# Kernel optimization log

Measured on AMD Instinct MI355X. Metric: run time of the kernel, lower is better.

The kernel has to match this reference:

```python
import jax, jax.numpy as jnp
import numpy as np

N = 100000   # nodes
E = 1600000  # edges
F = 128      # num_features
H = 128      # embedding_size
C = 10       # num_classes
G = 64       # graphs in batch


def setup_inputs() -> dict:
    key = jax.random.key(0)
    ks = jax.random.split(key, 10)
    x = jax.random.normal(ks[0], (N, F), jnp.float32)
    edge_index = jax.random.randint(ks[1], (2, E), 0, N)
    batch_index = jnp.sort(jax.random.randint(ks[2], (N,), 0, G))
    glorot = lambda k, shape: jax.random.normal(k, shape, jnp.float32) / np.float32(np.sqrt(shape[0]))
    return {
        "x": x, "edge_index": edge_index, "batch_index": batch_index,
        "W0": glorot(ks[3], (F, H)), "b0": jnp.zeros((H,), jnp.float32),
        "W1": glorot(ks[4], (H, H)), "b1": jnp.zeros((H,), jnp.float32),
        "W2": glorot(ks[5], (H, H)), "b2": jnp.zeros((H,), jnp.float32),
        "W3": glorot(ks[6], (H, H)), "b3": jnp.zeros((H,), jnp.float32),
        "Wout": glorot(ks[7], (2 * H, C)), "bout": jnp.zeros((C,), jnp.float32),
    }


def gcn_conv(x, W, b, src, dst):
    """PyG GCNConv: self-loops + symmetric D^-1/2 (A+I) D^-1/2 normalization."""
    n = x.shape[0]
    # degree with self-loop: deg[i] = 1 + in-degree(i)
    deg = 1.0 + jax.ops.segment_sum(jnp.ones(dst.shape[0], x.dtype), dst, num_segments=n)
    dinv = jax.lax.rsqrt(deg)
    h = x @ W  # [N, H]
    norm = (dinv[src] * dinv[dst])[:, None]  # [E, 1]
    agg = jax.ops.segment_sum(h[src] * norm, dst, num_segments=n)  # scatter-add over edges
    agg = agg + h * (1.0 / deg)[:, None]  # self-loop contribution dinv[i]^2 * h[i]
    return agg + b


def reference(x, edge_index, batch_index, W0, b0, W1, b1, W2, b2, W3, b3, Wout, bout):
    src, dst = edge_index[0], edge_index[1]
    h = jnp.tanh(gcn_conv(x, W0, b0, src, dst))
    h = jnp.tanh(gcn_conv(h, W1, b1, src, dst))
    h = jnp.tanh(gcn_conv(h, W2, b2, src, dst))
    h = jnp.tanh(gcn_conv(h, W3, b3, src, dst))
    # global max pool + global mean pool over batch_index
    gmax = jax.ops.segment_max(h, batch_index, num_segments=G)
    cnt = jax.ops.segment_sum(jnp.ones((h.shape[0],), h.dtype), batch_index, num_segments=G)
    gmean = jax.ops.segment_sum(h, batch_index, num_segments=G) / jnp.maximum(cnt, 1.0)[:, None]
    pooled = jnp.concatenate([gmax, gmean], axis=1)  # [G, 2H]
    out = pooled @ Wout + bout  # [G, C]
    return out, pooled
```

## Files before the change

kernel.cpp:

```cpp
#include <hip/hip_runtime.h>
#include <hip/hip_fp16.h>
#include <cmath>

typedef __attribute__((ext_vector_type(8))) short short8;
typedef __attribute__((ext_vector_type(8))) unsigned short ushort8;
typedef __attribute__((ext_vector_type(8))) _Float16 f16x8;
typedef __attribute__((ext_vector_type(4))) float f32x4;

#define MAXDEG 64

__device__ __forceinline__ unsigned pk_bf16(float a, float b) {
  unsigned r;
  asm("v_cvt_pk_bf16_f32 %0, %1, %2" : "=v"(r) : "v"(a), "v"(b));
  return r;
}

__device__ __forceinline__ float fast_tanh(float x) {
  float e2 = __expf(2.0f * x);
  return 1.0f - 2.0f * __builtin_amdgcn_rcpf(e2 + 1.0f);
}

#define FM_LO(A, U, W) \
  asm("v_fma_mix_f32 %0, %1, %2, %0 op_sel_hi:[1,0,0]" : "+v"(A) : "v"(U), "v"(W))
#define FM_HI(A, U, W) \
  asm("v_fma_mix_f32 %0, %1, %2, %0 op_sel:[1,0,0] op_sel_hi:[1,0,0]" : "+v"(A) : "v"(U), "v"(W))


__global__ __launch_bounds__(256) void count_fill(
    const int* __restrict__ src, const int* __restrict__ dst,
    unsigned* __restrict__ cnt, int* __restrict__ col, int E, int ncnt,
    const float* __restrict__ W0, const float* __restrict__ W1,
    const float* __restrict__ W2, const float* __restrict__ W3,
    unsigned short* __restrict__ Wt0Hi, unsigned short* __restrict__ Wt0Lo,
    unsigned short* __restrict__ WfHi, unsigned short* __restrict__ WfLo) {
  int b = blockIdx.x;
  if (b < ncnt) {
    int e = b * 256 + threadIdx.x;
    if (e < E) {
      int d = dst[e];
      unsigned pos = atomicAdd(&cnt[d], 1u);
      if (pos < MAXDEG) col[(d << 6) + (int)pos] = src[e];
    }
    return;
  }
  int t = (b - ncnt) * 256 + threadIdx.x;
  int l = t >> 13;
  int idx = t & 8191;
  const float* W = (l == 0) ? W0 : (l == 1) ? W1 : (l == 2) ? W2 : W3;
  int n = idx & 127, k = (idx >> 7) * 2;
  float w0 = W[k * 128 + n], w1 = W[(k + 1) * 128 + n];
  if (l == 0) {
    unsigned h01 = pk_bf16(w0, w1);
    float hf0 = __uint_as_float(h01 << 16);
    float hf1 = __uint_as_float(h01 & 0xFFFF0000u);
    unsigned l01 = pk_bf16(w0 - hf0, w1 - hf1);
    *(unsigned*)&Wt0Hi[n * 128 + k] = h01;
    *(unsigned*)&Wt0Lo[n * 128 + k] = l01;
  } else {
    __half2 hh = __float22half2_rn(make_float2(w0, w1));
    float r0 = __low2float(hh), r1 = __high2float(hh);
    __half2 ll = __float22half2_rn(make_float2((w0 - r0) * 1024.0f,
                                               (w1 - r1) * 1024.0f));
    *(__half2*)&WfHi[(l - 1) * 16384 + n * 128 + k] = hh;
    *(__half2*)&WfLo[(l - 1) * 16384 + n * 128 + k] = ll;
  }
}


__global__ __launch_bounds__(512) void prep_k(const unsigned* __restrict__ cnt,
                                              float* __restrict__ dinv,
                                              const int* __restrict__ batch,
                                              int* __restrict__ gstart, int n,
                                              int G) {
  int gid = blockIdx.x * 512 + threadIdx.x;
  if (gid < n) dinv[gid] = rsqrtf(1.0f + (float)cnt[gid]);
  if (blockIdx.x == 0 && threadIdx.x <= (unsigned)G) {
    int t = threadIdx.x;
    int lo = 0, hi = n;
    while (lo < hi) {
      int mid = (lo + hi) >> 1;
      if (batch[mid] < t) lo = mid + 1;
      else hi = mid;
    }
    gstart[t] = lo;
  }
}


#define LDK 136

__global__ __launch_bounds__(256) void gemm_mfma(const float* __restrict__ A,
                                                 const unsigned short* __restrict__ WtHi,
                                                 const unsigned short* __restrict__ WtLo,
                                                 const float* __restrict__ dinv,
                                                 __half* __restrict__ O, int M) {
  __shared__ unsigned short sHi[128 * LDK];
  __shared__ unsigned short sLo[128 * LDK];
  int tid = threadIdx.x;
#pragma unroll
  for (int i = 0; i < 8; ++i) {
    int c = tid + i * 256;
    int n = c >> 4;
    int off = (c & 15) * 8;
    *(ushort8*)&sHi[n * LDK + off] = *(const ushort8*)&WtHi[c * 8];
    *(ushort8*)&sLo[n * LDK + off] = *(const ushort8*)&WtLo[c * 8];
  }
  __syncthreads();

  int wv = tid >> 6, lane = tid & 63;
  int r0 = blockIdx.x * 128 + wv * 32;
  int lrow = lane & 15, lk = (lane >> 4) * 8;

  f32x4 acc[2][8] = {};
#pragma unroll
  for (int kk = 0; kk < 4; ++kk) {
    int k0 = kk * 32 + lk;
    short8 ahi[2], alo[2];
#pragma unroll
    for (int fr = 0; fr < 2; ++fr) {
      int row = r0 + fr * 16 + lrow;
      row = row < M ? row : M - 1;
      const float* ap = &A[(size_t)row * 128 + k0];
      float4 a0 = *(const float4*)ap;
      float4 a1 = *(const float4*)(ap + 4);
      union { short8 v; unsigned u32[4]; } h_, l_;
#define SPLIT2(slot, x, y)                              \
      {                                                 \
        unsigned hh = pk_bf16((x), (y));                \
        h_.u32[slot] = hh;                              \
        float hf0 = __uint_as_float(hh << 16);          \
        float hf1 = __uint_as_float(hh & 0xFFFF0000u);  \
        l_.u32[slot] = pk_bf16((x) - hf0, (y) - hf1);   \
      }
      SPLIT2(0, a0.x, a0.y)
      SPLIT2(1, a0.z, a0.w)
      SPLIT2(2, a1.x, a1.y)
      SPLIT2(3, a1.z, a1.w)
#undef SPLIT2
      ahi[fr] = h_.v;
      alo[fr] = l_.v;
    }
#pragma unroll
    for (int c = 0; c < 8; ++c) {
      int bidx = (c * 16 + lrow) * LDK + k0;
      short8 bhi = *(const short8*)&sHi[bidx];
      short8 blo = *(const short8*)&sLo[bidx];
#pragma unroll
      for (int fr = 0; fr < 2; ++fr) {
        acc[fr][c] = __builtin_amdgcn_mfma_f32_16x16x32_bf16(ahi[fr], bhi, acc[fr][c], 0, 0, 0);
        acc[fr][c] = __builtin_amdgcn_mfma_f32_16x16x32_bf16(ahi[fr], blo, acc[fr][c], 0, 0, 0);
        acc[fr][c] = __builtin_amdgcn_mfma_f32_16x16x32_bf16(alo[fr], bhi, acc[fr][c], 0, 0, 0);
      }
    }
  }
#pragma unroll
  for (int fr = 0; fr < 2; ++fr) {
#pragma unroll
    for (int r = 0; r < 4; ++r) {
      int row = r0 + fr * 16 + (lane >> 4) * 4 + r;
      if (row < M) {
        float dv = dinv[row];
#pragma unroll
        for (int c = 0; c < 8; ++c)
          O[(size_t)row * 128 + c * 16 + (lane & 15)] =
              __float2half(acc[fr][c][r] * dv);
      }
    }
  }
}


__global__ __launch_bounds__(256) void gemm_f16(const __half* __restrict__ Hf,
                                                const unsigned short* __restrict__ Whi,
                                                const unsigned short* __restrict__ Wlo,
                                                const float* __restrict__ dinv,
                                                __half* __restrict__ O, int M) {
  __shared__ unsigned short sHi[128 * LDK];
  __shared__ unsigned short sLo[128 * LDK];
  int tid = threadIdx.x;
#pragma unroll
  for (int i = 0; i < 8; ++i) {
    int c = tid + i * 256;
    int n = c >> 4;
    int off = (c & 15) * 8;
    *(ushort8*)&sHi[n * LDK + off] = *(const ushort8*)&Whi[c * 8];
    *(ushort8*)&sLo[n * LDK + off] = *(const ushort8*)&Wlo[c * 8];
  }
  __syncthreads();

  int wv = tid >> 6, lane = tid & 63;
  int r0 = blockIdx.x * 128 + wv * 32;
  int lrow = lane & 15, lk = (lane >> 4) * 8;

  f32x4 acc[2][8] = {};
  f32x4 accL[2][8] = {};
#pragma unroll
  for (int kk = 0; kk < 4; ++kk) {
    int k0 = kk * 32 + lk;
    f16x8 a[2];
#pragma unroll
    for (int fr = 0; fr < 2; ++fr) {
      int row = r0 + fr * 16 + lrow;
      row = row < M ? row : M - 1;
      a[fr] = *(const f16x8*)&Hf[(size_t)row * 128 + k0];
    }
#pragma unroll
    for (int c = 0; c < 8; ++c) {
      int bidx = (c * 16 + lrow) * LDK + k0;
      f16x8 bhi = *(const f16x8*)&sHi[bidx];
      f16x8 blo = *(const f16x8*)&sLo[bidx];
#pragma unroll
      for (int fr = 0; fr < 2; ++fr) {
        acc[fr][c] = __builtin_amdgcn_mfma_f32_16x16x32_f16(a[fr], bhi, acc[fr][c], 0, 0, 0);
        accL[fr][c] = __builtin_amdgcn_mfma_f32_16x16x32_f16(a[fr], blo, accL[fr][c], 0, 0, 0);
      }
    }
  }
  const float ls = 1.0f / 1024.0f;
#pragma unroll
  for (int fr = 0; fr < 2; ++fr) {
#pragma unroll
    for (int r = 0; r < 4; ++r) {
      int row = r0 + fr * 16 + (lane >> 4) * 4 + r;
      if (row < M) {
        float dv = dinv[row];
#pragma unroll
        for (int c = 0; c < 8; ++c)
          O[(size_t)row * 128 + c * 16 + (lane & 15)] =
              __float2half((acc[fr][c][r] + accL[fr][c][r] * ls) * dv);
      }
    }
  }
}


__global__ __launch_bounds__(256) void gather_k(const __half* __restrict__ h,
                                                const unsigned* __restrict__ cnt,
                                                const int* __restrict__ col,
                                                const float* __restrict__ dinv,
                                                const float* __restrict__ bias,
                                                __half* __restrict__ Hf, int N) {
  int wid = (int)((blockIdx.x * (size_t)blockDim.x + threadIdx.x) >> 6);
  if (wid >= N) return;
  int lane = threadIdx.x & 63;
  int grp = lane >> 4;
  int li = lane & 15;
  int deg = (int)cnt[wid];
  deg = deg < MAXDEG ? deg : MAXDEG;
  int s = wid << 6;
  int end = s + deg;
  const uint4* hrow = (const uint4*)h;

  float ac[8] = {};
  int niter = (deg + 15) >> 4;
  int base = s + grp;
#define ACC(U, W)                                        \
  {                                                      \
    FM_LO(ac[0], (U).x, (W)); FM_HI(ac[1], (U).x, (W));  \
    FM_LO(ac[2], (U).y, (W)); FM_HI(ac[3], (U).y, (W));  \
    FM_LO(ac[4], (U).z, (W)); FM_HI(ac[5], (U).z, (W));  \
    FM_LO(ac[6], (U).w, (W)); FM_HI(ac[7], (U).w, (W));  \
  }
  for (int it = 0; it < niter; ++it, base += 16) {
    int p0 = base, p1 = base + 4, p2 = base + 8, p3 = base + 12;
    int c0 = p0 < end ? p0 : s, c1 = p1 < end ? p1 : s;
    int c2 = p2 < end ? p2 : s, c3 = p3 < end ? p3 : s;
    int i0 = __builtin_nontemporal_load(&col[c0]);
    int i1 = __builtin_nontemporal_load(&col[c1]);
    int i2 = __builtin_nontemporal_load(&col[c2]);
    int i3 = __builtin_nontemporal_load(&col[c3]);
    float w0 = p0 < end ? 1.0f : 0.0f;
    float w1 = p1 < end ? 1.0f : 0.0f;
    float w2 = p2 < end ? 1.0f : 0.0f;
    float w3 = p3 < end ? 1.0f : 0.0f;
    uint4 v0 = hrow[(size_t)i0 * 16 + li];
    uint4 v1 = hrow[(size_t)i1 * 16 + li];
    uint4 v2 = hrow[(size_t)i2 * 16 + li];
    uint4 v3 = hrow[(size_t)i3 * 16 + li];
    ACC(v0, w0) ACC(v1, w1) ACC(v2, w2) ACC(v3, w3)
  }
#undef ACC
#pragma unroll
  for (int j = 0; j < 8; ++j) {
    ac[j] += __shfl_xor(ac[j], 16);
    ac[j] += __shfl_xor(ac[j], 32);
  }

  float a0 = grp == 0 ? ac[0] : grp == 1 ? ac[2] : grp == 2 ? ac[4] : ac[6];
  float a1 = grp == 0 ? ac[1] : grp == 1 ? ac[3] : grp == 2 ? ac[5] : ac[7];

  float dv = dinv[wid];
  uint4 sv = hrow[(size_t)wid * 16 + li];
  unsigned su = grp == 0 ? sv.x : grp == 1 ? sv.y : grp == 2 ? sv.z : sv.w;
  float2 sj = __half22float2(*(__half2*)&su);
  float2 bj = *(const float2*)&bias[li * 8 + 2 * grp];
  float o0 = fast_tanh(dv * (a0 + sj.x) + bj.x);
  float o1 = fast_tanh(dv * (a1 + sj.y) + bj.y);

  __half2 hv = __float22half2_rn(make_float2(o0, o1));
  *(__half2*)&Hf[(size_t)wid * 128 + li * 8 + 2 * grp] = hv;
}


#define CH 16

__global__ __launch_bounds__(128) void pool_partial(const __half* __restrict__ Hf,
                                                    const int* __restrict__ gstart,
                                                    float* __restrict__ pmax,
                                                    float* __restrict__ psum) {
  int g = blockIdx.x, c = blockIdx.y, f = threadIdx.x;
  int s = gstart[g], e = gstart[g + 1];
  long long len = e - s;
  int cs = s + (int)(len * c / CH);
  int ce = s + (int)(len * (c + 1) / CH);
  float m = -INFINITY, sum = 0.f;
  for (int n = cs; n < ce; ++n) {
    float v = __half2float(Hf[(size_t)n * 128 + f]);
    m = fmaxf(m, v);
    sum += v;
  }
  pmax[((size_t)g * CH + c) * 128 + f] = m;
  psum[((size_t)g * CH + c) * 128 + f] = sum;
}

__global__ __launch_bounds__(128) void pool_head(const float* __restrict__ pmax,
                                                 const float* __restrict__ psum,
                                                 const int* __restrict__ gstart,
                                                 const float* __restrict__ Wout,
                                                 const float* __restrict__ bout,
                                                 float* __restrict__ out, int G) {
  __shared__ float pl[256];
  int g = blockIdx.x, f = threadIdx.x;
  float m = -INFINITY, s = 0.f;
  for (int c = 0; c < CH; ++c) {
    m = fmaxf(m, pmax[((size_t)g * CH + c) * 128 + f]);
    s += psum[((size_t)g * CH + c) * 128 + f];
  }
  int cnt = gstart[g + 1] - gstart[g];
  float mean = s / fmaxf((float)cnt, 1.0f);
  float* pooled = out + (size_t)G * 10;
  pooled[(size_t)g * 256 + f] = m;
  pooled[(size_t)g * 256 + 128 + f] = mean;
  pl[f] = m;
  pl[128 + f] = mean;
  __syncthreads();
  if (f < 10) {
    float acc = bout[f];
    for (int k = 0; k < 256; ++k) acc += pl[k] * Wout[k * 10 + f];
    out[(size_t)g * 10 + f] = acc;
  }
}


extern "C" void kernel_launch(void* const* d_in, const int* in_sizes, int n_in,
                              void* d_out, int out_size, void* d_ws, size_t ws_size,
                              hipStream_t stream) {
  const float* x = (const float*)d_in[0];
  const int* ei = (const int*)d_in[1];
  const int* batch = (const int*)d_in[2];
  const float* W[4] = {(const float*)d_in[3], (const float*)d_in[5],
                       (const float*)d_in[7], (const float*)d_in[9]};
  const float* Bz[4] = {(const float*)d_in[4], (const float*)d_in[6],
                        (const float*)d_in[8], (const float*)d_in[10]};
  const float* Wout = (const float*)d_in[11];
  const float* bout = (const float*)d_in[12];
  const int N = in_sizes[0] / 128;
  const int E = in_sizes[1] / 2;
  const int G = 64;
  const int* srcp = ei;
  const int* dstp = ei + E;
  float* out = (float*)d_out;

  char* wsb = (char*)d_ws;
  size_t off = 0;
  auto alloc = [&](size_t bytes) -> void* {
    void* p = wsb + off;
    off = (off + bytes + 255) & ~(size_t)255;
    return p;
  };
  __half* bufA = (__half*)alloc((size_t)N * 128 * 2);
  __half* Hf = (__half*)alloc((size_t)N * 128 * 2);
  size_t cnt_off = off;
  unsigned* cnt = (unsigned*)alloc((size_t)N * 4);
  size_t cnt_span = off - cnt_off;
  int* col = (int*)alloc((size_t)N * MAXDEG * 4);
  float* dinv = (float*)alloc((size_t)N * 4);
  int* gstart = (int*)alloc(4096);
  float* pmax = (float*)alloc((size_t)G * CH * 128 * 4);
  float* psum = (float*)alloc((size_t)G * CH * 128 * 4);
  unsigned short* Wt0Hi = (unsigned short*)alloc(16384 * 2);
  unsigned short* Wt0Lo = (unsigned short*)alloc(16384 * 2);
  unsigned short* WfHi = (unsigned short*)alloc(3 * 16384 * 2);
  unsigned short* WfLo = (unsigned short*)alloc(3 * 16384 * 2);
  if (off > ws_size) return;

  hipMemsetAsync(wsb + cnt_off, 0, cnt_span, stream);

  int ncnt = (E + 255) / 256;
  count_fill<<<ncnt + 128, 256, 0, stream>>>(srcp, dstp, cnt, col, E, ncnt, W[0],
                                             W[1], W[2], W[3], Wt0Hi, Wt0Lo,
                                             WfHi, WfLo);
  prep_k<<<(N + 511) / 512, 512, 0, stream>>>(cnt, dinv, batch, gstart, N, G);

  int ggrid = (int)(((size_t)N * 64 + 255) / 256);
  for (int l = 0; l < 4; ++l) {
    if (l == 0)
      gemm_mfma<<<(N + 127) / 128, 256, 0, stream>>>(x, Wt0Hi, Wt0Lo, dinv, bufA, N);
    else
      gemm_f16<<<(N + 127) / 128, 256, 0, stream>>>(Hf, WfHi + (l - 1) * 16384,
                                                    WfLo + (l - 1) * 16384, dinv,
                                                    bufA, N);
    gather_k<<<ggrid, 256, 0, stream>>>(bufA, cnt, col, dinv, Bz[l], Hf, N);
  }

  pool_partial<<<dim3(G, CH), 128, 0, stream>>>(Hf, gstart, pmax, psum);
  pool_head<<<G, 128, 0, stream>>>(pmax, psum, gstart, Wout, bout, out, G);
}
```

Baseline: 507.5 us.

## Store node features in column-slab layout and split gather by feature slab

```diff
diff --git a/kernel.cpp b/kernel.cpp
--- a/kernel.cpp
+++ b/kernel.cpp
@@ -162,7 +162,7 @@
         float dv = dinv[row];
 #pragma unroll
         for (int c = 0; c < 8; ++c)
-          O[(size_t)row * 128 + c * 16 + (lane & 15)] =
+          O[((size_t)c * M + row) * 16 + (lane & 15)] =
               __float2half(acc[fr][c][r] * dv);
       }
     }
@@ -202,7 +202,7 @@
     for (int fr = 0; fr < 2; ++fr) {
       int row = r0 + fr * 16 + lrow;
       row = row < M ? row : M - 1;
-      a[fr] = *(const f16x8*)&Hf[(size_t)row * 128 + k0];
+      a[fr] = *(const f16x8*)&Hf[(((size_t)(k0 >> 4)) * M + row) * 16 + (k0 & 15)];
     }
 #pragma unroll
     for (int c = 0; c < 8; ++c) {
@@ -226,7 +226,7 @@
         float dv = dinv[row];
 #pragma unroll
         for (int c = 0; c < 8; ++c)
-          O[(size_t)row * 128 + c * 16 + (lane & 15)] =
+          O[((size_t)c * M + row) * 16 + (lane & 15)] =
               __float2half((acc[fr][c][r] + accL[fr][c][r] * ls) * dv);
       }
     }
@@ -240,65 +240,44 @@
                                                 const float* __restrict__ dinv,
                                                 const float* __restrict__ bias,
                                                 __half* __restrict__ Hf, int N) {
-  int wid = (int)((blockIdx.x * (size_t)blockDim.x + threadIdx.x) >> 6);
-  if (wid >= N) return;
+  int s = blockIdx.x & 7;
+  int nd = ((blockIdx.x >> 3) << 2) + (threadIdx.x >> 6);
+  if (nd >= N) return;
   int lane = threadIdx.x & 63;
-  int grp = lane >> 4;
-  int li = lane & 15;
-  int deg = (int)cnt[wid];
+  int grp = lane >> 3;
+  int li = lane & 7;
+  int deg = (int)cnt[nd];
   deg = deg < MAXDEG ? deg : MAXDEG;
-  int s = wid << 6;
-  int end = s + deg;
-  const uint4* hrow = (const uint4*)h;
-
-  float ac[8] = {};
+  int colv = (lane < deg) ? col[(nd << 6) + lane] : nd;
+  const unsigned* hs = (const unsigned*)h + (size_t)s * N * 8;
+
+  float a0 = 0.f, a1 = 0.f;
   int niter = (deg + 15) >> 4;
-  int base = s + grp;
-#define ACC(U, W)                                        \
-  {                                                      \
-    FM_LO(ac[0], (U).x, (W)); FM_HI(ac[1], (U).x, (W));  \
-    FM_LO(ac[2], (U).y, (W)); FM_HI(ac[3], (U).y, (W));  \
-    FM_LO(ac[4], (U).z, (W)); FM_HI(ac[5], (U).z, (W));  \
-    FM_LO(ac[6], (U).w, (W)); FM_HI(ac[7], (U).w, (W));  \
-  }
-  for (int it = 0; it < niter; ++it, base += 16) {
-    int p0 = base, p1 = base + 4, p2 = base + 8, p3 = base + 12;
-    int c0 = p0 < end ? p0 : s, c1 = p1 < end ? p1 : s;
-    int c2 = p2 < end ? p2 : s, c3 = p3 < end ? p3 : s;
-    int i0 = __builtin_nontemporal_load(&col[c0]);
-    int i1 = __builtin_nontemporal_load(&col[c1]);
-    int i2 = __builtin_nontemporal_load(&col[c2]);
-    int i3 = __builtin_nontemporal_load(&col[c3]);
-    float w0 = p0 < end ? 1.0f : 0.0f;
-    float w1 = p1 < end ? 1.0f : 0.0f;
-    float w2 = p2 < end ? 1.0f : 0.0f;
-    float w3 = p3 < end ? 1.0f : 0.0f;
-    uint4 v0 = hrow[(size_t)i0 * 16 + li];
-    uint4 v1 = hrow[(size_t)i1 * 16 + li];
-    uint4 v2 = hrow[(size_t)i2 * 16 + li];
-    uint4 v3 = hrow[(size_t)i3 * 16 + li];
-    ACC(v0, w0) ACC(v1, w1) ACC(v2, w2) ACC(v3, w3)
-  }
-#undef ACC
-#pragma unroll
-  for (int j = 0; j < 8; ++j) {
-    ac[j] += __shfl_xor(ac[j], 16);
-    ac[j] += __shfl_xor(ac[j], 32);
-  }
-
-  float a0 = grp == 0 ? ac[0] : grp == 1 ? ac[2] : grp == 2 ? ac[4] : ac[6];
-  float a1 = grp == 0 ? ac[1] : grp == 1 ? ac[3] : grp == 2 ? ac[5] : ac[7];
-
-  float dv = dinv[wid];
-  uint4 sv = hrow[(size_t)wid * 16 + li];
-  unsigned su = grp == 0 ? sv.x : grp == 1 ? sv.y : grp == 2 ? sv.z : sv.w;
+  for (int it = 0; it < niter; ++it) {
+    int e0 = it * 16 + grp, e1 = e0 + 8;
+    int i0 = __shfl(colv, e0);
+    int i1 = __shfl(colv, e1);
+    float w0 = e0 < deg ? 1.0f : 0.0f;
+    float w1 = e1 < deg ? 1.0f : 0.0f;
+    unsigned v0 = hs[(size_t)i0 * 8 + li];
+    unsigned v1 = hs[(size_t)i1 * 8 + li];
+    FM_LO(a0, v0, w0); FM_HI(a1, v0, w0);
+    FM_LO(a0, v1, w1); FM_HI(a1, v1, w1);
+  }
+  a0 += __shfl_xor(a0, 8);  a1 += __shfl_xor(a1, 8);
+  a0 += __shfl_xor(a0, 16); a1 += __shfl_xor(a1, 16);
+  a0 += __shfl_xor(a0, 32); a1 += __shfl_xor(a1, 32);
+
+  float dv = dinv[nd];
+  unsigned su = hs[(size_t)nd * 8 + li];
   float2 sj = __half22float2(*(__half2*)&su);
-  float2 bj = *(const float2*)&bias[li * 8 + 2 * grp];
+  float2 bj = *(const float2*)&bias[s * 16 + li * 2];
   float o0 = fast_tanh(dv * (a0 + sj.x) + bj.x);
   float o1 = fast_tanh(dv * (a1 + sj.y) + bj.y);
-
-  __half2 hv = __float22half2_rn(make_float2(o0, o1));
-  *(__half2*)&Hf[(size_t)wid * 128 + li * 8 + 2 * grp] = hv;
+  if (grp == 0) {
+    __half2 hv = __float22half2_rn(make_float2(o0, o1));
+    *(__half2*)&Hf[((size_t)s * N + nd) * 16 + li * 2] = hv;
+  }
 }
 
 
@@ -307,15 +286,16 @@
 __global__ __launch_bounds__(128) void pool_partial(const __half* __restrict__ Hf,
                                                     const int* __restrict__ gstart,
                                                     float* __restrict__ pmax,
-                                                    float* __restrict__ psum) {
+                                                    float* __restrict__ psum, int N) {
   int g = blockIdx.x, c = blockIdx.y, f = threadIdx.x;
   int s = gstart[g], e = gstart[g + 1];
   long long len = e - s;
   int cs = s + (int)(len * c / CH);
   int ce = s + (int)(len * (c + 1) / CH);
+  const __half* base = Hf + ((size_t)(f >> 4)) * N * 16 + (f & 15);
   float m = -INFINITY, sum = 0.f;
   for (int n = cs; n < ce; ++n) {
-    float v = __half2float(Hf[(size_t)n * 128 + f]);
+    float v = __half2float(base[(size_t)n * 16]);
     m = fmaxf(m, v);
     sum += v;
   }
@@ -402,7 +382,7 @@
                                              WfHi, WfLo);
   prep_k<<<(N + 511) / 512, 512, 0, stream>>>(cnt, dinv, batch, gstart, N, G);
 
-  int ggrid = (int)(((size_t)N * 64 + 255) / 256);
+  int ggrid = 8 * ((N + 3) / 4);
   for (int l = 0; l < 4; ++l) {
     if (l == 0)
       gemm_mfma<<<(N + 127) / 128, 256, 0, stream>>>(x, Wt0Hi, Wt0Lo, dinv, bufA, N);
@@ -413,6 +393,6 @@
     gather_k<<<ggrid, 256, 0, stream>>>(bufA, cnt, col, dinv, Bz[l], Hf, N);
   }
 
-  pool_partial<<<dim3(G, CH), 128, 0, stream>>>(Hf, gstart, pmax, psum);
+  pool_partial<<<dim3(G, CH), 128, 0, stream>>>(Hf, gstart, pmax, psum, N);
   pool_head<<<G, 128, 0, stream>>>(pmax, psum, gstart, Wout, bout, out, G);
 }
```

New measurement: 1.029 ms. 2.03x slower.
